# Kernel optimization log

Hardware: AMD Instinct MI355X
Metric: run time of the kernel (lower is better)

Reference implementation:

```python
import jax, jax.numpy as jnp
import numpy as np

D_BINS = 59          # cfg.cam_d
BEV_H, BEV_W = 128, 128


def setup_inputs() -> dict:
    key = jax.random.key(0)
    k = jax.random.split(key, 7)
    B, N, Cin, H, W = 4, 6, 256, 16, 44
    C = 80  # cfg.cam_bev_c
    img_feats = jax.random.normal(k[0], (B, N, Cin, H, W), dtype=jnp.float32)
    rots = jax.random.normal(k[1], (B, N, 3, 3), dtype=jnp.float32)
    trans = jax.random.normal(k[2], (B, N, 3), dtype=jnp.float32)
    intrins = jax.random.normal(k[3], (B, N, 3, 3), dtype=jnp.float32)
    # 1x1 conv == per-pixel linear layer: weight (D+C, Cin), bias (D+C,)
    w_depth = jax.random.normal(k[4], (D_BINS + C, Cin), dtype=jnp.float32) / np.sqrt(Cin)
    b_depth = jnp.zeros((D_BINS + C,), dtype=jnp.float32)
    # projected BEV grid indices (what get_geometry produces via randint)
    geom = jax.random.randint(k[5], (B, N, D_BINS, H, W, 2), 0, BEV_H, dtype=jnp.int32)
    return {"img_feats": img_feats, "rots": rots, "trans": trans,
            "intrins": intrins, "w_depth": w_depth, "b_depth": b_depth,
            "geom": geom}


def reference(img_feats, rots, trans, intrins, w_depth, b_depth, geom):
    B, N, Cin, H, W = img_feats.shape
    C = w_depth.shape[0] - D_BINS
    # depth_net: 1x1 conv -> (B, N, D+C, H, W)
    x = jnp.einsum('bnchw,oc->bnohw', img_feats, w_depth) + b_depth[None, None, :, None, None]
    depth = jax.nn.softmax(x[:, :, :D_BINS], axis=2)          # (B,N,D,H,W)
    context = x[:, :, D_BINS:]                                 # (B,N,C,H,W)
    # outer product: (B,N,D,C,H,W) -> (B,N,D,H,W,C)
    frustum = depth[:, :, :, None] * context[:, :, None]
    frustum = jnp.transpose(frustum, (0, 1, 2, 4, 5, 3))
    # voxel pooling: scatter-add frustum points into BEV grid by geom indices
    cell = geom[..., 0] * BEV_W + geom[..., 1]                 # (B,N,D,H,W)
    flat_idx = (jnp.arange(B, dtype=jnp.int32)[:, None] * (BEV_H * BEV_W)
                + cell.reshape(B, -1)).reshape(-1)
    bev = jax.ops.segment_sum(frustum.reshape(-1, C), flat_idx,
                              num_segments=B * BEV_H * BEV_W)
    return bev.reshape(B, BEV_H, BEV_W, C).transpose(0, 3, 1, 2)  # (B,C,bev_h,bev_w)
```

## Files before the change

kernel.cpp:

```cpp
#include <hip/hip_runtime.h>
#include <hip/hip_bf16.h>
#include <math.h>

#define D_BINS 59
#define CTX    80
#define O_TOT  139
#define K_CIN  256
#define PIXELS 704
#define BNPAIR 24
#define BEVHW  16384
#define NBATCH 4

#define NTILE   128
#define NBUCKET (NBATCH * NTILE)
#define TCELLS  128

#define PXT    16
#define NPXT   44
#define NBLK   (BNPAIR * NPXT)
#define SEGS   (6 * NPXT)
#define EPB    (PXT * D_BINS)

#define CAP    2816
#define CAPP   (CAP + TCELLS * 7)

#define WHL_OFF    0
#define WHL_F      36864
#define CTX_OFF    (WHL_OFF + WHL_F)
#define CTX_F      (BNPAIR * PIXELS * CTX / 2)
#define CNTMAT_OFF (CTX_OFF + CTX_F)
#define OFSMAT_OFF (CNTMAT_OFF + NBLK * NTILE)
#define PLIST_OFF  (OFSMAT_OFF + NBLK * NTILE)

typedef __attribute__((ext_vector_type(8))) short bf16x8;
typedef __attribute__((ext_vector_type(4))) float f32x4;

__device__ __forceinline__ unsigned short f2bf(float v) {
    __hip_bfloat16 h = __float2bfloat16(v);
    return *reinterpret_cast<unsigned short*>(&h);
}
__device__ __forceinline__ float bf2f(unsigned short u) {
    return __uint_as_float(((unsigned)u) << 16);
}

__global__ __launch_bounds__(256) void wsplit_kernel(
    const float* __restrict__ w, unsigned short* __restrict__ whl)
{
    const int row = blockIdx.x;
    const int col = threadIdx.x;
    const float v = (row < O_TOT) ? w[(size_t)row * K_CIN + col] : 0.f;
    const unsigned short hi = f2bf(v);
    const unsigned short lo = f2bf(v - bf2f(hi));
    whl[row * K_CIN + col]         = hi;
    whl[36864 + row * K_CIN + col] = lo;
}

template<int NT, int T0>
__device__ __forceinline__ void kloop(
    const float* __restrict__ ib, const unsigned short* __restrict__ whl,
    int pxg, int m, int g, f32x4* acc)
{
#pragma unroll 2
    for (int ks = 0; ks < 8; ++ks) {
        float bv[8];
#pragma unroll
        for (int j = 0; j < 8; ++j)
            bv[j] = ib[(size_t)(ks * 32 + 8 * g + j) * PIXELS + pxg];
        bf16x8 bhi, blo;
#pragma unroll
        for (int j = 0; j < 8; ++j) {
            const unsigned short h = f2bf(bv[j]);
            bhi[j] = (short)h;
            blo[j] = (short)f2bf(bv[j] - bf2f(h));
        }
#pragma unroll
        for (int t = 0; t < NT; ++t) {
            const int row = (T0 + t) * 16 + m;
            const bf16x8 ahi = *(const bf16x8*)&whl[(size_t)row * K_CIN + ks * 32 + g * 8];
            const bf16x8 alo = *(const bf16x8*)&whl[36864 + (size_t)row * K_CIN + ks * 32 + g * 8];
            acc[t] = __builtin_amdgcn_mfma_f32_16x16x32_bf16(ahi, bhi, acc[t], 0, 0, 0);
            acc[t] = __builtin_amdgcn_mfma_f32_16x16x32_bf16(ahi, blo, acc[t], 0, 0, 0);
            acc[t] = __builtin_amdgcn_mfma_f32_16x16x32_bf16(alo, bhi, acc[t], 0, 0, 0);
        }
    }
}

__global__ __launch_bounds__(64) void gemm_fused(
    const float* __restrict__ img,
    const unsigned short* __restrict__ whl,
    const float* __restrict__ bias,
    const int*   __restrict__ geom,
    __hip_bfloat16* __restrict__ ctx,
    uint2*       __restrict__ plist,
    int*         __restrict__ cntmat,
    int*         __restrict__ ofsmat)
{
    const int lane = threadIdx.x;
    const int m    = lane & 15;
    const int g    = lane >> 4;
    const int pt   = blockIdx.x;
    const int bn   = blockIdx.y;
    const int p0   = pt * PXT;
    const int pxg  = p0 + m;
    const int blkid = bn * NPXT + pt;
    const float* ib = img + (size_t)bn * K_CIN * PIXELS;

    if (blockIdx.z == 0) {
        __shared__ int lh[NTILE], lofs[NTILE], lcur[NTILE];
        f32x4 acc[4];
#pragma unroll
        for (int t = 0; t < 4; ++t) acc[t] = (f32x4){0.f, 0.f, 0.f, 0.f};
        kloop<4, 0>(ib, whl, pxg, m, g, acc);

        const int2* g2 = (const int2*)geom;
        int2 gg[4][4];
#pragma unroll
        for (int t = 0; t < 4; ++t)
#pragma unroll
            for (int r = 0; r < 4; ++r) {
                const int o = 16 * t + 4 * g + r;
                if (o < D_BINS)
                    gg[t][r] = g2[((size_t)(bn * D_BINS + o)) * PIXELS + pxg];
            }
        lh[lane] = 0; lh[lane + 64] = 0;
        lcur[lane] = 0; lcur[lane + 64] = 0;

#pragma unroll
        for (int t = 0; t < 4; ++t)
#pragma unroll
            for (int r = 0; r < 4; ++r) acc[t][r] += bias[16 * t + 4 * g + r];

        float gm = -INFINITY;
#pragma unroll
        for (int t = 0; t < 4; ++t)
#pragma unroll
            for (int r = 0; r < 4; ++r)
                if (16 * t + 4 * g + r < D_BINS) gm = fmaxf(gm, acc[t][r]);
        gm = fmaxf(gm, __shfl_xor(gm, 16));
        gm = fmaxf(gm, __shfl_xor(gm, 32));
        float ls = 0.f;
#pragma unroll
        for (int t = 0; t < 4; ++t)
#pragma unroll
            for (int r = 0; r < 4; ++r)
                if (16 * t + 4 * g + r < D_BINS) {
                    const float e = __expf(acc[t][r] - gm);
                    acc[t][r] = e;
                    ls += e;
                }
        ls += __shfl_xor(ls, 16);
        ls += __shfl_xor(ls, 32);
        const float inv = 1.f / ls;

        unsigned uc[4][4];
#pragma unroll
        for (int t = 0; t < 4; ++t)
#pragma unroll
            for (int r = 0; r < 4; ++r) {
                const int o = 16 * t + 4 * g + r;
                if (o < D_BINS) {
                    const int2 q = gg[t][r];
                    const int tile = (q.x >> 3) * 8 + (q.y >> 4);
                    const int cell = (q.x & 7) * 16 + (q.y & 15);
                    uc[t][r] = (unsigned)((tile << 7) | cell);
                    atomicAdd(&lh[tile], 1);
                }
            }

        const int l2 = 2 * lane;
        const int a = lh[l2];
        const int b = lh[l2 + 1];
        const int p = a + b;
        int incl = p;
#pragma unroll
        for (int off = 1; off < 64; off <<= 1) {
            const int t = __shfl_up(incl, off);
            if (lane >= off) incl += t;
        }
        const int excl = incl - p;
        lofs[l2]     = excl;
        lofs[l2 + 1] = excl + a;
        *(int2*)&cntmat[(size_t)blkid * NTILE + l2] = make_int2(a, b);
        *(int2*)&ofsmat[(size_t)blkid * NTILE + l2] = make_int2(excl, excl + a);

        uint2* dst = plist + (size_t)blkid * EPB;
        const unsigned ctxoff = (unsigned)((bn * PIXELS + pxg) * CTX);
#pragma unroll
        for (int t = 0; t < 4; ++t)
#pragma unroll
            for (int r = 0; r < 4; ++r) {
                const int o = 16 * t + 4 * g + r;
                if (o < D_BINS) {
                    const unsigned u = uc[t][r];
                    const int tl = (int)(u >> 7);
                    const int pos = lofs[tl] + atomicAdd(&lcur[tl], 1);
                    dst[pos] = make_uint2(__float_as_uint(acc[t][r] * inv),
                                          (ctxoff << 7) | (u & 127u));
                }
            }
    } else {
        __shared__ unsigned short sctx[PXT][CTX];
        f32x4 acc[6];
#pragma unroll
        for (int t = 0; t < 6; ++t) acc[t] = (f32x4){0.f, 0.f, 0.f, 0.f};
        kloop<6, 3>(ib, whl, pxg, m, g, acc);

#pragma unroll
        for (int t = 0; t < 6; ++t)
#pragma unroll
            for (int r = 0; r < 4; ++r) {
                const int o = (3 + t) * 16 + 4 * g + r;
                const int c = o - D_BINS;
                if (c >= 0 && c < CTX)
                    sctx[m][c] = f2bf(acc[t][r] + bias[o]);
            }
        const char* sb = (const char*)sctx;
        char* gb = (char*)ctx + ((size_t)(bn * PIXELS) + p0) * CTX * 2;
#pragma unroll
        for (int i = lane; i < PXT * CTX * 2 / 16; i += 64)
            *(float4*)(gb + i * 16) = *(const float4*)(sb + i * 16);
    }
}

__global__ __launch_bounds__(1024) void gather_kernel(
    const uint2* __restrict__ plist,
    const int*   __restrict__ cntmat,
    const int*   __restrict__ ofsmat,
    const unsigned short* __restrict__ ctx,
    float*       __restrict__ out)
{
    __shared__ float sacc[CTX][TCELLS + 1];
    __shared__ uint2 bufB[CAPP];
    __shared__ int sg[512];
    __shared__ int segcnt[SEGS], segofs[SEGS];
    __shared__ int cellcnt[TCELLS], celloff[TCELLS], cellcur[TCELLS], sc[TCELLS];
    uint2* bufA = (uint2*)sacc;

    const int tid    = threadIdx.x;
    const int wv     = tid >> 6;
    const int lane   = tid & 63;
    const int bucket = blockIdx.x;
    const int b      = bucket >> 7;
    const int tile   = bucket & 127;
    const int blk0   = b * SEGS;

    if (tid < 512) {
        const int c = (tid < SEGS) ? cntmat[(size_t)(blk0 + tid) * NTILE + tile] : 0;
        sg[tid] = c;
        if (tid < SEGS) segcnt[tid] = c;
    }
    __syncthreads();
#pragma unroll
    for (int off = 1; off < 512; off <<= 1) {
        const int t = (tid < 512 && tid >= off) ? sg[tid - off] : 0;
        __syncthreads();
        if (tid < 512) sg[tid] += t;
        __syncthreads();
    }
    if (tid < SEGS) segofs[tid] = sg[tid] - segcnt[tid];
    __syncthreads();
    const int total = sg[511];

    {
        const int sub = lane >> 3;
        const int sl  = lane & 7;
        for (int sgi = wv * 8 + sub; sgi < SEGS; sgi += 128) {
            const int n = segcnt[sgi];
            if (!n) continue;
            const int dstb = segofs[sgi];
            const uint2* sp = plist + (size_t)(blk0 + sgi) * EPB
                              + ofsmat[(size_t)(blk0 + sgi) * NTILE + tile];
            for (int i = sl; i < n; i += 8) {
                const int d = dstb + i;
                if (d < CAP) bufA[d] = sp[i];
            }
        }
    }
    const int ncap = (total < CAP) ? total : CAP;
    __syncthreads();

    if (tid < TCELLS) cellcnt[tid] = 0;
    __syncthreads();
    for (int i = tid; i < ncap; i += 1024)
        atomicAdd(&cellcnt[bufA[i].y & 127u], 1);
    __syncthreads();
    if (tid < TCELLS) sc[tid] = (cellcnt[tid] + 7) & ~7;
    __syncthreads();
#pragma unroll
    for (int off = 1; off < TCELLS; off <<= 1) {
        const int t = (tid < TCELLS && tid >= off) ? sc[tid - off] : 0;
        __syncthreads();
        if (tid < TCELLS) sc[tid] += t;
        __syncthreads();
    }
    if (tid < TCELLS) {
        celloff[tid] = sc[tid] - ((cellcnt[tid] + 7) & ~7);
        cellcur[tid] = 0;
    }
    __syncthreads();
    const int padtotal = sc[TCELLS - 1];
    for (int i = tid; i < padtotal; i += 1024) bufB[i] = make_uint2(0u, 0u);
    __syncthreads();
    for (int i = tid; i < ncap; i += 1024) {
        const uint2 e = bufA[i];
        const int c = (int)(e.y & 127u);
        bufB[celloff[c] + atomicAdd(&cellcur[c], 1)] = e;
    }
    __syncthreads();

    for (int c = wv; c < TCELLS; c += 16) {
        const int s0 = celloff[c];
        const int pc = (cellcnt[c] + 7) & ~7;
        float a0 = 0.f, a1 = 0.f;
        for (int i = 0; i < pc; i += 8) {
            uint2 e[8];
#pragma unroll
            for (int r = 0; r < 8; ++r) e[r] = bufB[s0 + i + r];
            if (lane < 40) {
                unsigned u[8];
#pragma unroll
                for (int r = 0; r < 8; ++r)
                    u[r] = *(const unsigned*)(ctx + (e[r].y >> 7) + 2 * lane);
#pragma unroll
                for (int r = 0; r < 8; ++r) {
                    const float d  = __uint_as_float(e[r].x);
                    a0 += d * __uint_as_float(u[r] << 16);
                    a1 += d * __uint_as_float(u[r] & 0xffff0000u);
                }
            }
        }
        if (lane < 40) {
            sacc[2 * lane][c]     = a0;
            sacc[2 * lane + 1][c] = a1;
        }
    }

    if (total > CAP) {
        for (int sgi = 0; sgi < SEGS; ++sgi) {
            const int dstb = segofs[sgi];
            const int n    = segcnt[sgi];
            if (dstb + n <= CAP) continue;
            const uint2* sp = plist + (size_t)(blk0 + sgi) * EPB
                              + ofsmat[(size_t)(blk0 + sgi) * NTILE + tile];
            const int i0 = (CAP > dstb) ? (CAP - dstb) : 0;
            for (int i = i0; i < n; ++i) {
                const uint2 e = sp[i];
                const int c = (int)(e.y & 127u);
                if ((c & 15) == wv && lane < 40) {
                    const unsigned u = *(const unsigned*)(ctx + (e.y >> 7) + 2 * lane);
                    const float dep = __uint_as_float(e.x);
                    sacc[2 * lane][c]     += dep * __uint_as_float(u << 16);
                    sacc[2 * lane + 1][c] += dep * __uint_as_float(u & 0xffff0000u);
                }
            }
        }
    }
    __syncthreads();

    const int tl = bucket & 127;
    const int tr = tl >> 3;
    const int tc = tl & 7;
    const int c0  = tid >> 4;
    const int col = tid & 15;
#pragma unroll
    for (int cc = c0; cc < CTX; cc += 64) {
#pragma unroll
        for (int r = 0; r < 8; ++r) {
            out[((size_t)(b * CTX + cc)) * BEVHW + (tr * 8 + r) * 128 + tc * 16 + col]
                = sacc[cc][r * 16 + col];
        }
    }
}

extern "C" void kernel_launch(void* const* d_in, const int* in_sizes, int n_in,
                              void* d_out, int out_size, void* d_ws, size_t ws_size,
                              hipStream_t stream)
{
    const float* img  = (const float*)d_in[0];
    const float* w    = (const float*)d_in[4];
    const float* bias = (const float*)d_in[5];
    const int*   geom = (const int*)d_in[6];
    float*       out  = (float*)d_out;

    float* ws = (float*)d_ws;
    unsigned short* whl = (unsigned short*)(ws + WHL_OFF);
    __hip_bfloat16* ctx = (__hip_bfloat16*)(ws + CTX_OFF);
    int*   cntmat = (int*)(ws + CNTMAT_OFF);
    int*   ofsmat = (int*)(ws + OFSMAT_OFF);
    uint2* plist  = (uint2*)(ws + PLIST_OFF);

    wsplit_kernel<<<144, 256, 0, stream>>>(w, whl);

    {
        dim3 grid(NPXT, BNPAIR, 2);
        gemm_fused<<<grid, 64, 0, stream>>>(img, whl, bias, geom, ctx,
                                            plist, cntmat, ofsmat);
    }

    gather_kernel<<<NBUCKET, 1024, 0, stream>>>(plist, cntmat, ofsmat,
                                                (const unsigned short*)ctx, out);
}
```

Measured before the change: 140.6 us.

## Precompute per-cell histograms globally and scatter directly into cell-sorted shared buffer

The GEMM kernel now atomically builds a global per-bucket cell histogram, which the weight-split kernel zeroes. This lets the gather kernel compute cell offsets up front and scatter entries straight from global memory into a cell-sorted shared buffer. That removes the intermediate bufA copy, the shared-memory count pass and the block-wide 512-element scan. The count and offset matrices are transposed for coalesced reads in gather, the GEMM k-loop gains software prefetch of the next B slice, and bias loads are vectorized and hoisted. The cost is global atomics in the GEMM kernel and a slow fallback path when a bucket exceeds shared capacity.

```diff
diff --git a/kernel.cpp b/kernel.cpp
--- a/kernel.cpp
+++ b/kernel.cpp
@@ -24,13 +24,14 @@
 #define CAP    2816
 #define CAPP   (CAP + TCELLS * 7)
 
-#define WHL_OFF    0
-#define WHL_F      36864
-#define CTX_OFF    (WHL_OFF + WHL_F)
-#define CTX_F      (BNPAIR * PIXELS * CTX / 2)
-#define CNTMAT_OFF (CTX_OFF + CTX_F)
-#define OFSMAT_OFF (CNTMAT_OFF + NBLK * NTILE)
-#define PLIST_OFF  (OFSMAT_OFF + NBLK * NTILE)
+#define WHL_OFF      0
+#define WHL_F        36864
+#define CTX_OFF      (WHL_OFF + WHL_F)
+#define CTX_F        (BNPAIR * PIXELS * CTX / 2)
+#define CNTMAT_OFF   (CTX_OFF + CTX_F)
+#define OFSMAT_OFF   (CNTMAT_OFF + NTILE * NBLK)
+#define CELLHIST_OFF (OFSMAT_OFF + NTILE * NBLK)
+#define PLIST_OFF    (CELLHIST_OFF + NBUCKET * TCELLS)
 
 typedef __attribute__((ext_vector_type(8))) short bf16x8;
 typedef __attribute__((ext_vector_type(4))) float f32x4;
@@ -44,7 +45,8 @@
 }
 
 __global__ __launch_bounds__(256) void wsplit_kernel(
-    const float* __restrict__ w, unsigned short* __restrict__ whl)
+    const float* __restrict__ w, unsigned short* __restrict__ whl,
+    int* __restrict__ cellhist)
 {
     const int row = blockIdx.x;
     const int col = threadIdx.x;
@@ -53,6 +55,8 @@
     const unsigned short lo = f2bf(v - bf2f(hi));
     whl[row * K_CIN + col]         = hi;
     whl[36864 + row * K_CIN + col] = lo;
+    const int zid = blockIdx.x * 256 + threadIdx.x;
+    for (int i = zid; i < NBUCKET * TCELLS; i += 144 * 256) cellhist[i] = 0;
 }
 
 template<int NT, int T0>
@@ -60,12 +64,18 @@
     const float* __restrict__ ib, const unsigned short* __restrict__ whl,
     int pxg, int m, int g, f32x4* acc)
 {
-#pragma unroll 2
+    const float* bp = ib + (size_t)(8 * g) * PIXELS + pxg;
+    float bv[8];
+#pragma unroll
+    for (int j = 0; j < 8; ++j) bv[j] = bp[(size_t)j * PIXELS];
+#pragma unroll
     for (int ks = 0; ks < 8; ++ks) {
-        float bv[8];
-#pragma unroll
-        for (int j = 0; j < 8; ++j)
-            bv[j] = ib[(size_t)(ks * 32 + 8 * g + j) * PIXELS + pxg];
+        float bvn[8];
+        if (ks < 7) {
+#pragma unroll
+            for (int j = 0; j < 8; ++j)
+                bvn[j] = bp[(size_t)((ks + 1) * 32 + j) * PIXELS];
+        }
         bf16x8 bhi, blo;
 #pragma unroll
         for (int j = 0; j < 8; ++j) {
@@ -82,6 +92,10 @@
             acc[t] = __builtin_amdgcn_mfma_f32_16x16x32_bf16(ahi, blo, acc[t], 0, 0, 0);
             acc[t] = __builtin_amdgcn_mfma_f32_16x16x32_bf16(alo, bhi, acc[t], 0, 0, 0);
         }
+        if (ks < 7) {
+#pragma unroll
+            for (int j = 0; j < 8; ++j) bv[j] = bvn[j];
+        }
     }
 }
 
@@ -92,8 +106,9 @@
     const int*   __restrict__ geom,
     __hip_bfloat16* __restrict__ ctx,
     uint2*       __restrict__ plist,
-    int*         __restrict__ cntmat,
-    int*         __restrict__ ofsmat)
+    int*         __restrict__ cntmat_t,
+    int*         __restrict__ ofsmat_t,
+    int*         __restrict__ cellhist)
 {
     const int lane = threadIdx.x;
     const int m    = lane & 15;
@@ -107,28 +122,33 @@
 
     if (blockIdx.z == 0) {
         __shared__ int lh[NTILE], lofs[NTILE], lcur[NTILE];
-        f32x4 acc[4];
-#pragma unroll
-        for (int t = 0; t < 4; ++t) acc[t] = (f32x4){0.f, 0.f, 0.f, 0.f};
-        kloop<4, 0>(ib, whl, pxg, m, g, acc);
 
         const int2* g2 = (const int2*)geom;
         int2 gg[4][4];
-#pragma unroll
-        for (int t = 0; t < 4; ++t)
+        float4 bb[4];
+#pragma unroll
+        for (int t = 0; t < 4; ++t) {
+            bb[t] = *(const float4*)&bias[16 * t + 4 * g];
 #pragma unroll
             for (int r = 0; r < 4; ++r) {
                 const int o = 16 * t + 4 * g + r;
                 if (o < D_BINS)
                     gg[t][r] = g2[((size_t)(bn * D_BINS + o)) * PIXELS + pxg];
             }
+        }
         lh[lane] = 0; lh[lane + 64] = 0;
         lcur[lane] = 0; lcur[lane + 64] = 0;
 
-#pragma unroll
-        for (int t = 0; t < 4; ++t)
-#pragma unroll
-            for (int r = 0; r < 4; ++r) acc[t][r] += bias[16 * t + 4 * g + r];
+        f32x4 acc[4];
+#pragma unroll
+        for (int t = 0; t < 4; ++t) acc[t] = (f32x4){0.f, 0.f, 0.f, 0.f};
+        kloop<4, 0>(ib, whl, pxg, m, g, acc);
+
+#pragma unroll
+        for (int t = 0; t < 4; ++t) {
+            acc[t][0] += bb[t].x; acc[t][1] += bb[t].y;
+            acc[t][2] += bb[t].z; acc[t][3] += bb[t].w;
+        }
 
         float gm = -INFINITY;
 #pragma unroll
@@ -152,6 +172,7 @@
         ls += __shfl_xor(ls, 32);
         const float inv = 1.f / ls;
 
+        const int bat = bn / 6;
         unsigned uc[4][4];
 #pragma unroll
         for (int t = 0; t < 4; ++t)
@@ -164,6 +185,7 @@
                     const int cell = (q.x & 7) * 16 + (q.y & 15);
                     uc[t][r] = (unsigned)((tile << 7) | cell);
                     atomicAdd(&lh[tile], 1);
+                    atomicAdd(&cellhist[(bat << 14) | uc[t][r]], 1);
                 }
             }
 
@@ -180,8 +202,10 @@
         const int excl = incl - p;
         lofs[l2]     = excl;
         lofs[l2 + 1] = excl + a;
-        *(int2*)&cntmat[(size_t)blkid * NTILE + l2] = make_int2(a, b);
-        *(int2*)&ofsmat[(size_t)blkid * NTILE + l2] = make_int2(excl, excl + a);
+        cntmat_t[(size_t)l2 * NBLK + blkid]       = a;
+        cntmat_t[(size_t)(l2 + 1) * NBLK + blkid] = b;
+        ofsmat_t[(size_t)l2 * NBLK + blkid]       = excl;
+        ofsmat_t[(size_t)(l2 + 1) * NBLK + blkid] = excl + a;
 
         uint2* dst = plist + (size_t)blkid * EPB;
         const unsigned ctxoff = (unsigned)((bn * PIXELS + pxg) * CTX);
@@ -200,20 +224,27 @@
             }
     } else {
         __shared__ unsigned short sctx[PXT][CTX];
+        float4 bb[6];
+#pragma unroll
+        for (int t = 0; t < 6; ++t)
+            bb[t] = *(const float4*)&bias[(3 + t) * 16 + 4 * g];
+
         f32x4 acc[6];
 #pragma unroll
         for (int t = 0; t < 6; ++t) acc[t] = (f32x4){0.f, 0.f, 0.f, 0.f};
         kloop<6, 3>(ib, whl, pxg, m, g, acc);
 
 #pragma unroll
-        for (int t = 0; t < 6; ++t)
+        for (int t = 0; t < 6; ++t) {
+            const float bvv[4] = {bb[t].x, bb[t].y, bb[t].z, bb[t].w};
 #pragma unroll
             for (int r = 0; r < 4; ++r) {
                 const int o = (3 + t) * 16 + 4 * g + r;
                 const int c = o - D_BINS;
                 if (c >= 0 && c < CTX)
-                    sctx[m][c] = f2bf(acc[t][r] + bias[o]);
-            }
+                    sctx[m][c] = f2bf(acc[t][r] + bvv[r]);
+            }
+        }
         const char* sb = (const char*)sctx;
         char* gb = (char*)ctx + ((size_t)(bn * PIXELS) + p0) * CTX * 2;
 #pragma unroll
@@ -224,17 +255,17 @@
 
 __global__ __launch_bounds__(1024) void gather_kernel(
     const uint2* __restrict__ plist,
-    const int*   __restrict__ cntmat,
-    const int*   __restrict__ ofsmat,
+    const int*   __restrict__ cntmat_t,
+    const int*   __restrict__ ofsmat_t,
+    const int*   __restrict__ cellhist,
     const unsigned short* __restrict__ ctx,
     float*       __restrict__ out)
 {
     __shared__ float sacc[CTX][TCELLS + 1];
     __shared__ uint2 bufB[CAPP];
-    __shared__ int sg[512];
-    __shared__ int segcnt[SEGS], segofs[SEGS];
-    __shared__ int cellcnt[TCELLS], celloff[TCELLS], cellcur[TCELLS], sc[TCELLS];
-    uint2* bufA = (uint2*)sacc;
+    __shared__ int segcnt[SEGS], segofsG[SEGS];
+    __shared__ int cellcnt[TCELLS], celloff[TCELLS], cellcur[TCELLS];
+    __shared__ int sPadTotal;
 
     const int tid    = threadIdx.x;
     const int wv     = tid >> 6;
@@ -244,106 +275,92 @@
     const int tile   = bucket & 127;
     const int blk0   = b * SEGS;
 
-    if (tid < 512) {
-        const int c = (tid < SEGS) ? cntmat[(size_t)(blk0 + tid) * NTILE + tile] : 0;
-        sg[tid] = c;
-        if (tid < SEGS) segcnt[tid] = c;
-    }
+    if (tid < SEGS) {
+        segcnt[tid]  = cntmat_t[(size_t)tile * NBLK + blk0 + tid];
+        segofsG[tid] = ofsmat_t[(size_t)tile * NBLK + blk0 + tid];
+    }
+    if (tid >= 512 && tid < 512 + TCELLS)
+        cellcnt[tid - 512] = cellhist[(size_t)bucket * TCELLS + (tid - 512)];
     __syncthreads();
-#pragma unroll
-    for (int off = 1; off < 512; off <<= 1) {
-        const int t = (tid < 512 && tid >= off) ? sg[tid - off] : 0;
+
+    if (wv == 1) {
+        int carry = 0;
+#pragma unroll
+        for (int c = 0; c < 2; ++c) {
+            const int i = c * 64 + lane;
+            const int pv = (cellcnt[i] + 7) & ~7;
+            int incl = pv;
+#pragma unroll
+            for (int off = 1; off < 64; off <<= 1) {
+                const int t = __shfl_up(incl, off);
+                if (lane >= off) incl += t;
+            }
+            celloff[i] = carry + incl - pv;
+            cellcur[i] = 0;
+            carry += __shfl(incl, 63);
+        }
+        if (lane == 0) sPadTotal = carry;
+    }
+    __syncthreads();
+    const int padtotal = sPadTotal;
+
+    if (padtotal <= CAPP) {
+        if (tid < TCELLS) {
+            const int o = celloff[tid] + cellcnt[tid];
+            const int e = celloff[tid] + ((cellcnt[tid] + 7) & ~7);
+            for (int i = o; i < e; ++i) bufB[i] = make_uint2(0u, 0u);
+        }
+        {
+            const int sub = lane >> 3;
+            const int sl  = lane & 7;
+            for (int sgi = wv * 8 + sub; sgi < SEGS; sgi += 128) {
+                const int n = segcnt[sgi];
+                if (!n) continue;
+                const uint2* sp = plist + (size_t)(blk0 + sgi) * EPB + segofsG[sgi];
+                for (int i = sl; i < n; i += 8) {
+                    const uint2 e = sp[i];
+                    const int c = (int)(e.y & 127u);
+                    bufB[celloff[c] + atomicAdd(&cellcur[c], 1)] = e;
+                }
+            }
+        }
         __syncthreads();
-        if (tid < 512) sg[tid] += t;
+
+        for (int c = wv; c < TCELLS; c += 16) {
+            const int s0 = celloff[c];
+            const int pc = (cellcnt[c] + 7) & ~7;
+            float a0 = 0.f, a1 = 0.f;
+            for (int i = 0; i < pc; i += 8) {
+                uint2 e[8];
+#pragma unroll
+                for (int r = 0; r < 8; ++r) e[r] = bufB[s0 + i + r];
+                if (lane < 40) {
+                    unsigned u[8];
+#pragma unroll
+                    for (int r = 0; r < 8; ++r)
+                        u[r] = *(const unsigned*)(ctx + (e[r].y >> 7) + 2 * lane);
+#pragma unroll
+                    for (int r = 0; r < 8; ++r) {
+                        const float d  = __uint_as_float(e[r].x);
+                        a0 += d * __uint_as_float(u[r] << 16);
+                        a1 += d * __uint_as_float(u[r] & 0xffff0000u);
+                    }
+                }
+            }
+            if (lane < 40) {
+                sacc[2 * lane][c]     = a0;
+                sacc[2 * lane + 1][c] = a1;
+            }
+        }
+    } else {
+        for (int i = tid; i < CTX * (TCELLS + 1); i += 1024)
+            ((float*)sacc)[i] = 0.f;
         __syncthreads();
-    }
-    if (tid < SEGS) segofs[tid] = sg[tid] - segcnt[tid];
-    __syncthreads();
-    const int total = sg[511];
-
-    {
-        const int sub = lane >> 3;
-        const int sl  = lane & 7;
-        for (int sgi = wv * 8 + sub; sgi < SEGS; sgi += 128) {
+        for (int sgi = 0; sgi < SEGS; ++sgi) {
             const int n = segcnt[sgi];
             if (!n) continue;
-            const int dstb = segofs[sgi];
-            const uint2* sp = plist + (size_t)(blk0 + sgi) * EPB
-                              + ofsmat[(size_t)(blk0 + sgi) * NTILE + tile];
-            for (int i = sl; i < n; i += 8) {
-                const int d = dstb + i;
-                if (d < CAP) bufA[d] = sp[i];
-            }
-        }
-    }
-    const int ncap = (total < CAP) ? total : CAP;
-    __syncthreads();
-
-    if (tid < TCELLS) cellcnt[tid] = 0;
-    __syncthreads();
-    for (int i = tid; i < ncap; i += 1024)
-        atomicAdd(&cellcnt[bufA[i].y & 127u], 1);
-    __syncthreads();
-    if (tid < TCELLS) sc[tid] = (cellcnt[tid] + 7) & ~7;
-    __syncthreads();
-#pragma unroll
-    for (int off = 1; off < TCELLS; off <<= 1) {
-        const int t = (tid < TCELLS && tid >= off) ? sc[tid - off] : 0;
-        __syncthreads();
-        if (tid < TCELLS) sc[tid] += t;
-        __syncthreads();
-    }
-    if (tid < TCELLS) {
-        celloff[tid] = sc[tid] - ((cellcnt[tid] + 7) & ~7);
-        cellcur[tid] = 0;
-    }
-    __syncthreads();
-    const int padtotal = sc[TCELLS - 1];
-    for (int i = tid; i < padtotal; i += 1024) bufB[i] = make_uint2(0u, 0u);
-    __syncthreads();
-    for (int i = tid; i < ncap; i += 1024) {
-        const uint2 e = bufA[i];
-        const int c = (int)(e.y & 127u);
-        bufB[celloff[c] + atomicAdd(&cellcur[c], 1)] = e;
-    }
-    __syncthreads();
-
-    for (int c = wv; c < TCELLS; c += 16) {
-        const int s0 = celloff[c];
-        const int pc = (cellcnt[c] + 7) & ~7;
-        float a0 = 0.f, a1 = 0.f;
-        for (int i = 0; i < pc; i += 8) {
-            uint2 e[8];
-#pragma unroll
-            for (int r = 0; r < 8; ++r) e[r] = bufB[s0 + i + r];
-            if (lane < 40) {
-                unsigned u[8];
-#pragma unroll
-                for (int r = 0; r < 8; ++r)
-                    u[r] = *(const unsigned*)(ctx + (e[r].y >> 7) + 2 * lane);
-#pragma unroll
-                for (int r = 0; r < 8; ++r) {
-                    const float d  = __uint_as_float(e[r].x);
-                    a0 += d * __uint_as_float(u[r] << 16);
-                    a1 += d * __uint_as_float(u[r] & 0xffff0000u);
-                }
-            }
-        }
-        if (lane < 40) {
-            sacc[2 * lane][c]     = a0;
-            sacc[2 * lane + 1][c] = a1;
-        }
-    }
-
-    if (total > CAP) {
-        for (int sgi = 0; sgi < SEGS; ++sgi) {
-            const int dstb = segofs[sgi];
-            const int n    = segcnt[sgi];
-            if (dstb + n <= CAP) continue;
-            const uint2* sp = plist + (size_t)(blk0 + sgi) * EPB
-                              + ofsmat[(size_t)(blk0 + sgi) * NTILE + tile];
-            const int i0 = (CAP > dstb) ? (CAP - dstb) : 0;
-            for (int i = i0; i < n; ++i) {
+            const uint2* sp = plist + (size_t)(blk0 + sgi) * EPB + segofsG[sgi];
+            for (int i = 0; i < n; ++i) {
                 const uint2 e = sp[i];
                 const int c = (int)(e.y & 127u);
                 if ((c & 15) == wv && lane < 40) {
@@ -357,9 +374,8 @@
     }
     __syncthreads();
 
-    const int tl = bucket & 127;
-    const int tr = tl >> 3;
-    const int tc = tl & 7;
+    const int tr = tile >> 3;
+    const int tc = tile & 7;
     const int c0  = tid >> 4;
     const int col = tid & 15;
 #pragma unroll
@@ -385,18 +401,20 @@
     float* ws = (float*)d_ws;
     unsigned short* whl = (unsigned short*)(ws + WHL_OFF);
     __hip_bfloat16* ctx = (__hip_bfloat16*)(ws + CTX_OFF);
-    int*   cntmat = (int*)(ws + CNTMAT_OFF);
-    int*   ofsmat = (int*)(ws + OFSMAT_OFF);
-    uint2* plist  = (uint2*)(ws + PLIST_OFF);
-
-    wsplit_kernel<<<144, 256, 0, stream>>>(w, whl);
+    int*   cntmat_t = (int*)(ws + CNTMAT_OFF);
+    int*   ofsmat_t = (int*)(ws + OFSMAT_OFF);
+    int*   cellhist = (int*)(ws + CELLHIST_OFF);
+    uint2* plist    = (uint2*)(ws + PLIST_OFF);
+
+    wsplit_kernel<<<144, 256, 0, stream>>>(w, whl, cellhist);
 
     {
         dim3 grid(NPXT, BNPAIR, 2);
         gemm_fused<<<grid, 64, 0, stream>>>(img, whl, bias, geom, ctx,
-                                            plist, cntmat, ofsmat);
-    }
-
-    gather_kernel<<<NBUCKET, 1024, 0, stream>>>(plist, cntmat, ofsmat,
+                                            plist, cntmat_t, ofsmat_t, cellhist);
+    }
+
+    gather_kernel<<<NBUCKET, 1024, 0, stream>>>(plist, cntmat_t, ofsmat_t,
+                                                cellhist,
                                                 (const unsigned short*)ctx, out);
 }
```

Result: slower. 173.5 us (+23.4%).
